# Performance work log

Hardware: AMD Instinct MI355X
Metric: run time of the kernel (lower is better)

## Reference

```python
import jax, jax.numpy as jnp
import numpy as np

E, H, N, HD, HID = 8, 12, 256, 64, 512  # experts, heads, tokens, head_dim, hidden_dim
B, K = 32, 2                             # batch, top_k


def setup_inputs() -> dict:
    key = jax.random.key(0)
    ks = jax.random.split(key, 7)
    w = lambda k, shp: (jax.random.uniform(k, shp, jnp.float32) * 2.0 - 1.0) * 0.05  # kaiming-uniform-ish
    return {
        "x": jax.random.normal(ks[0], (B, H, HD, N), jnp.float32),
        "expert_indices": jax.random.randint(ks[1], (B, H, K), 0, E),
        "expert_weights": jax.random.uniform(ks[2], (B, H, K), dtype=jnp.float32),
        "fc1_tok": w(ks[3], (E, H, HID, N)),
        "fc1_chan": w(ks[4], (E, H, HD, HD)),
        "fc1_bias": jnp.zeros((E, H, HD, HID), jnp.float32),
        "fc2_tok": w(ks[5], (E, H, N, HID)),
        "fc2_chan": w(ks[6], (E, H, HD, HD)),
        "fc2_bias": jnp.zeros((E, H, HD, N), jnp.float32),
    }


def reference(x, expert_indices, expert_weights, fc1_tok, fc1_chan, fc1_bias,
              fc2_tok, fc2_chan, fc2_bias):
    # x: (B,H,hd,N); expert_indices/weights: (B,H,K)
    Bh, Hh = x.shape[0], x.shape[1]
    hidx = jnp.arange(Hh)[None, :, None]           # (1,H,1) broadcasts with (B,H,K)
    gather = lambda p: p[expert_indices, hidx]     # -> (B,H,K, ...)
    w1t, w1c, b1 = gather(fc1_tok), gather(fc1_chan), gather(fc1_bias)
    w2t, w2c, b2 = gather(fc2_tok), gather(fc2_chan), gather(fc2_bias)
    # Layer 1: h = GELU(W1_chan @ x @ W1_tok^T + B1)   (token mix then channel mix)
    h = jnp.einsum('bhdn,bhken->bhkde', x, w1t)        # (B,H,K,hd,hid)
    h = jnp.einsum('bhkcd,bhkde->bhkce', w1c, h) + b1
    h = jax.nn.gelu(h, approximate=True)               # tanh approximation
    # Layer 2: out = W2_chan @ h @ W2_tok^T + B2
    o = jnp.einsum('bhkde,bhkne->bhkdn', h, w2t)       # (B,H,K,hd,N)
    o = jnp.einsum('bhkcd,bhkdn->bhkcn', w2c, o) + b2
    # Weighted combine over top_k
    return jnp.einsum('bhkdn,bhk->bhdn', o, expert_weights)
```

## Files before the change

kernel.cpp:

```cpp
#include <hip/hip_runtime.h>
#include <hip/hip_bf16.h>


namespace {
constexpr int NHEAD = 12, NTOK = 256, HDIM = 64, HIDD = 512, NBATCH = 32, TOPK = 2;
constexpr int NCHAIN = NBATCH * NHEAD * TOPK;
constexpr int NBH = NBATCH * NHEAD;
constexpr int NGROUP = 8 * NHEAD;

constexpr int P_T1 = HDIM * 2 + 16;
constexpr int T1_W = 64 * P_T1;
constexpr int SMA_TOTAL = 4 * T1_W;
constexpr int P_T3 = HDIM * 2 + 16;
constexpr int T3_W = 64 * P_T3;
constexpr int SMB_TOTAL = 4 * T3_W;

constexpr size_t SZ_H    = (size_t)NCHAIN * HDIM * HIDD;
constexpr size_t OFF_H   = 0;
constexpr size_t OFF_W1T = OFF_H + SZ_H;
constexpr size_t SZ_W1T  = (size_t)8 * NHEAD * HIDD * NTOK;
constexpr size_t OFF_W2T = OFF_W1T + SZ_W1T;
constexpr size_t SZ_W2T  = (size_t)8 * NHEAD * NTOK * HIDD;
constexpr size_t OFF_X   = OFF_W2T + SZ_W2T;
constexpr size_t SZ_X    = (size_t)NBATCH * NHEAD * HDIM * NTOK;
constexpr size_t OFF_B1  = OFF_X + SZ_X;
constexpr size_t SZ_B1   = (size_t)8 * NHEAD * HDIM * HIDD;
constexpr size_t OFF_B2  = OFF_B1 + SZ_B1;
constexpr size_t SZ_B2   = (size_t)8 * NHEAD * HDIM * NTOK;
constexpr size_t OFF_W1C = OFF_B2 + SZ_B2;
constexpr size_t SZ_W1C  = (size_t)8 * NHEAD * HDIM * HDIM;
constexpr size_t OFF_W2C = OFF_W1C + SZ_W1C;
constexpr size_t SZ_W2C  = (size_t)8 * NHEAD * HDIM * HDIM;
constexpr size_t TOTEL   = OFF_W2C + SZ_W2C;
constexpr size_t NEED    = TOTEL * 2 + (NCHAIN + NBH) * 4;

constexpr int NB_W1T = (int)(SZ_W1T / (16 * 256));
constexpr int NB_W2T = (int)(SZ_W2T / (16 * 512));
constexpr int NB_X   = (int)(SZ_X   / (16 * 256));
constexpr int NB_W1C = (int)(SZ_W1C / (16 * 64));
constexpr int NB_W2C = (int)(SZ_W2C / (16 * 64));
constexpr int NB_B1  = (int)(SZ_B1  / (16 * 512));
constexpr int NB_B2  = (int)(SZ_B2  / (16 * 256));
constexpr int NB_TOT = NB_W1T + NB_W2T + NB_X + NB_W1C + NB_W2C + NB_B1 + NB_B2;
}

typedef float f32x4 __attribute__((ext_vector_type(4)));
typedef short bf16x8 __attribute__((ext_vector_type(8)));
typedef short bf16x4 __attribute__((ext_vector_type(4)));

#define MFMA16(a, b, c) __builtin_amdgcn_mfma_f32_16x16x32_bf16((a), (b), (c), 0, 0, 0)

#define GLOAD_LDS16(g, l)                                                  \
  __builtin_amdgcn_global_load_lds(                                        \
      (const __attribute__((address_space(1))) unsigned int*)(g),          \
      (__attribute__((address_space(3))) unsigned int*)(l), 16, 0, 0)

__device__ __forceinline__ short f2bf(float f) {
  union { float f; unsigned u; } v; v.f = f;
  unsigned r = v.u + 0x7fffu + ((v.u >> 16) & 1u);
  return (short)(r >> 16);
}

__device__ __forceinline__ bf16x8 ld_gfrag(const float* p) {
  float4 a = *(const float4*)p;
  float4 b = *(const float4*)(p + 4);
  bf16x8 r;
  r[0] = f2bf(a.x); r[1] = f2bf(a.y); r[2] = f2bf(a.z); r[3] = f2bf(a.w);
  r[4] = f2bf(b.x); r[5] = f2bf(b.y); r[6] = f2bf(b.z); r[7] = f2bf(b.w);
  return r;
}

__device__ __forceinline__ f32x4 bf4f(bf16x4 v) {
  f32x4 r;
  #pragma unroll
  for (int i = 0; i < 4; ++i) {
    union { unsigned u; float f; } t;
    t.u = ((unsigned)(unsigned short)v[i]) << 16;
    r[i] = t.f;
  }
  return r;
}

__device__ __forceinline__ float gelu_fast(float x) {
  float arg = -2.30220826f * x * __builtin_fmaf(0.044715f, x * x, 1.0f);
  float e = __builtin_amdgcn_exp2f(arg);
  return x * __builtin_amdgcn_rcpf(1.0f + e);
}

__device__ __forceinline__ int xcd_chunk(int bx, int nwg) {
  return (bx & 7) * (nwg >> 3) + (bx >> 3);
}

__device__ __forceinline__ int swz8(int c)  { return c ^ (((c >> 4) & 3) << 1); }

__global__ __launch_bounds__(256) void prepack_sort_kernel(
    const float* __restrict__ w1t, const float* __restrict__ w2t,
    const float* __restrict__ x, const float* __restrict__ w1c,
    const float* __restrict__ w2c, const float* __restrict__ b1,
    const float* __restrict__ b2, short* __restrict__ wsb,
    const int* __restrict__ eidx, int* __restrict__ order, int* __restrict__ order2) {
  if (blockIdx.x == 0) {
    __shared__ int keys[NCHAIN];
    __shared__ int keys2[NBH];
    __shared__ int cnt[NGROUP + 1];
    __shared__ int cnt2[NGROUP + 1];
    const int t = threadIdx.x;
    for (int i = t; i <= NGROUP; i += 256) { cnt[i] = 0; cnt2[i] = 0; }
    __syncthreads();
    for (int i = t; i < NCHAIN; i += 256) {
      int h = (i >> 1) % NHEAD;
      int key = eidx[i] * NHEAD + h;
      keys[i] = key;
      atomicAdd(&cnt[key + 1], 1);
    }
    for (int i = t; i < NBH; i += 256) {
      int h = i % NHEAD;
      int key = eidx[i * TOPK] * NHEAD + h;
      keys2[i] = key;
      atomicAdd(&cnt2[key + 1], 1);
    }
    __syncthreads();
    if (t == 0) for (int i = 1; i <= NGROUP; ++i) cnt[i] += cnt[i - 1];
    if (t == 1) for (int i = 1; i <= NGROUP; ++i) cnt2[i] += cnt2[i - 1];
    __syncthreads();
    for (int i = t; i < NCHAIN; i += 256) {
      int pos = atomicAdd(&cnt[keys[i]], 1);
      order[pos] = i;
    }
    for (int i = t; i < NBH; i += 256) {
      int pos = atomicAdd(&cnt2[keys2[i]], 1);
      order2[pos] = i;
    }
    __syncthreads();
  }

  __shared__ __align__(16) float tilef[8192];
  short* tile = (short*)tilef;

  const int w64 = (threadIdx.x >> 6) * 64;
  const int lane = threadIdx.x & 63;

  for (int band = blockIdx.x; band < NB_TOT; band += gridDim.x) {
    const float* s; size_t dbase; int R, rcSh, tprSh; bool g8;
    int bb = band;
    if (bb < NB_W1T)                 { s = w1t; dbase = OFF_W1T; R = 256; rcSh = 6; tprSh = 3; g8 = true; }
    else if ((bb -= NB_W1T) < NB_W2T){ s = w2t; dbase = OFF_W2T; R = 512; rcSh = 7; tprSh = 4; g8 = true; }
    else if ((bb -= NB_W2T) < NB_X)  { s = x;   dbase = OFF_X;   R = 256; rcSh = 6; tprSh = 3; g8 = true; }
    else if ((bb -= NB_X) < NB_W1C)  { s = w1c; dbase = OFF_W1C; R = 64;  rcSh = 4; tprSh = 1; g8 = true; }
    else if ((bb -= NB_W1C) < NB_W2C){ s = w2c; dbase = OFF_W2C; R = 64;  rcSh = 4; tprSh = 1; g8 = true; }
    else if ((bb -= NB_W2C) < NB_B1) { s = b1;  dbase = OFF_B1;  R = 512; rcSh = 7; tprSh = 5; g8 = false; }
    else                             { bb -= NB_B1; s = b2; dbase = OFF_B2; R = 256; rcSh = 6; tprSh = 4; g8 = false; }

    const size_t eloff = (size_t)bb * 16 * R;

    if (g8) {
      const int nc = 4 * R;
      const float* bs = s + eloff;
      for (int c0 = w64; c0 < nc; c0 += 256) {
        const int c = c0 + lane;
        const int row = c >> rcSh, cir = c & ((1 << rcSh) - 1);
        const float* g = bs + (((size_t)row << rcSh) + (cir ^ (row & 7))) * 4;
        GLOAD_LDS16(g, tilef + (size_t)c0 * 4);
      }
      __syncthreads();

      const int n8 = (16 * R) / 8;
      for (int l8 = threadIdx.x; l8 < n8; l8 += 256) {
        const int frag = l8 >> 6, l6 = l8 & 63;
        const int c8 = ((frag & ((1 << tprSh) - 1)) << 2) + (l6 >> 4);
        const int r  = ((frag >> tprSh) << 4) + (l6 & 15);
        const int ch0 = (r << rcSh) + ((2 * c8) ^ (r & 7));
        const int ch1 = (r << rcSh) + ((2 * c8 + 1) ^ (r & 7));
        f32x4 a = *(const f32x4*)(tilef + ch0 * 4);
        f32x4 b = *(const f32x4*)(tilef + ch1 * 4);
        bf16x8 v;
        #pragma unroll
        for (int i = 0; i < 4; ++i) { v[i] = f2bf(a[i]); v[4 + i] = f2bf(b[i]); }
        *(bf16x8*)(wsb + dbase + eloff + (size_t)l8 * 8) = v;
      }
    } else {
      const int n8 = (16 * R) / 8;
      for (int l8 = threadIdx.x; l8 < n8; l8 += 256) {
        const int l = l8 * 8;
        const int r = l >> rcSh >> 2, c = l & (R - 1);
        bf16x8 v = ld_gfrag(s + eloff + l);
        #pragma unroll
        for (int q = 0; q < 2; ++q) {
          const int e4 = (c >> 2) + q;
          const int chunk = (e4 >> 2) * 64 + (e4 & 3) * 16 + r;
          bf16x4 p;
          #pragma unroll
          for (int i = 0; i < 4; ++i) p[i] = v[q * 4 + i];
          *(bf16x4*)(tile + swz8(chunk) * 4) = p;
        }
      }
      __syncthreads();
      for (int l8 = threadIdx.x; l8 < n8; l8 += 256) {
        const int l4 = l8 * 2;
        bf16x8 v;
        bf16x4 a = *(const bf16x4*)(tile + swz8(l4) * 4);
        bf16x4 b = *(const bf16x4*)(tile + swz8(l4 + 1) * 4);
        #pragma unroll
        for (int i = 0; i < 4; ++i) { v[i] = a[i]; v[4 + i] = b[i]; }
        *(bf16x8*)(wsb + dbase + eloff + (size_t)l8 * 8) = v;
      }
    }
    __syncthreads();
  }
}

template <bool PP>
__global__ __launch_bounds__(256) void mixer_h_kernel(
    const float* __restrict__ x, const int* __restrict__ eidx,
    const float* __restrict__ w1t, const float* __restrict__ w1c, const float* __restrict__ b1,
    const short* __restrict__ wsb, const int* __restrict__ order, short* __restrict__ hws) {
  __shared__ __align__(16) char smem[SMA_TOTAL];
  const int L = xcd_chunk(blockIdx.x, NCHAIN * 2);
  const int sid = L >> 1, eblk = L & 1;
  const int bhk = PP ? order[sid] : sid;
  const int h = (bhk >> 1) % NHEAD;
  const int tid = threadIdx.x, w = tid >> 6, lane = tid & 63, lr = lane & 15, lg = lane >> 4;

  const int e = eidx[bhk];
  const size_t eh = (size_t)e * NHEAD + h;
  short* H = hws + (size_t)bhk * HDIM * HIDD;

  const int e0 = eblk * 256 + w * 64;
  const int et0 = e0 >> 4;
  const int ks0B = e0 >> 5;

  const short* W1Tp = wsb + OFF_W1T + (eh << 17);
  const short* Xp   = wsb + OFF_X + ((size_t)(bhk >> 1) << 14);
  const short* W1Cp = wsb + OFF_W1C + (eh << 12);
  const short* B1p  = wsb + OFF_B1 + (eh << 15);

  f32x4 acc1[4][4];
  #pragma unroll
  for (int et = 0; et < 4; ++et)
    #pragma unroll
    for (int dt = 0; dt < 4; ++dt) acc1[et][dt] = (f32x4){0.f, 0.f, 0.f, 0.f};
  #pragma unroll
  for (int ks = 0; ks < 8; ++ks) {
    bf16x8 wfr[4];
    #pragma unroll
    for (int et = 0; et < 4; ++et) {
      if (PP) wfr[et] = *(const bf16x8*)(W1Tp + (size_t)(((et0 + et) * 8 + ks) * 512) + lane * 8);
      else    wfr[et] = ld_gfrag(w1t + eh * HIDD * NTOK +
                                 (size_t)(e0 + et * 16 + lr) * NTOK + ks * 32 + lg * 8);
    }
    #pragma unroll
    for (int dt = 0; dt < 4; ++dt) {
      bf16x8 xfr;
      if (PP) xfr = *(const bf16x8*)(Xp + (size_t)((dt * 8 + ks) * 512) + lane * 8);
      else    xfr = ld_gfrag(x + (size_t)(bhk >> 1) * HDIM * NTOK +
                             (size_t)(dt * 16 + lr) * NTOK + ks * 32 + lg * 8);
      #pragma unroll
      for (int et = 0; et < 4; ++et) acc1[et][dt] = MFMA16(xfr, wfr[et], acc1[et][dt]);
    }
  }

  char* t1 = smem + w * T1_W;
  #pragma unroll
  for (int et = 0; et < 4; ++et)
    #pragma unroll
    for (int dt = 0; dt < 4; ++dt) {
      bf16x4 p;
      #pragma unroll
      for (int i = 0; i < 4; ++i) p[i] = f2bf(acc1[et][dt][i]);
      *(bf16x4*)(t1 + (et * 16 + lr) * P_T1 + (dt * 16 + lg * 4) * 2) = p;
    }

  f32x4 acc2[4][4];
  #pragma unroll
  for (int et = 0; et < 4; ++et)
    #pragma unroll
    for (int ct = 0; ct < 4; ++ct) {
      if (PP) {
        bf16x4 bb = *(const bf16x4*)(B1p + (size_t)((ct * 32 + et0 + et) * 256) + lane * 4);
        acc2[et][ct] = bf4f(bb);
      } else {
        acc2[et][ct] = *(const f32x4*)(b1 + eh * HDIM * HIDD +
                                       (size_t)(ct * 16 + lr) * HIDD + e0 + et * 16 + lg * 4);
      }
    }
  #pragma unroll
  for (int ks = 0; ks < 2; ++ks) {
    bf16x8 a[4];
    #pragma unroll
    for (int et = 0; et < 4; ++et)
      a[et] = *(const bf16x8*)(t1 + (et * 16 + lr) * P_T1 + (ks * 32 + lg * 8) * 2);
    #pragma unroll
    for (int ct = 0; ct < 4; ++ct) {
      bf16x8 bfr;
      if (PP) bfr = *(const bf16x8*)(W1Cp + (size_t)((ct * 2 + ks) * 512) + lane * 8);
      else    bfr = ld_gfrag(w1c + eh * HDIM * HDIM +
                             (size_t)(ct * 16 + lr) * HDIM + ks * 32 + lg * 8);
      #pragma unroll
      for (int et = 0; et < 4; ++et) acc2[et][ct] = MFMA16(a[et], bfr, acc2[et][ct]);
    }
  }

  #pragma unroll
  for (int et = 0; et < 4; ++et) {
    const int ksB = ks0B + (et >> 1);
    const int lgB = (et & 1) * 2 + (lg >> 1);
    #pragma unroll
    for (int ct = 0; ct < 4; ++ct) {
      bf16x4 g;
      #pragma unroll
      for (int i = 0; i < 4; ++i) g[i] = f2bf(gelu_fast(acc2[et][ct][i]));
      if (PP) {
        *(bf16x4*)(H + (size_t)((ct * 16 + ksB) * 512) + (lgB * 16 + lr) * 8 + (lg & 1) * 4) = g;
      } else {
        *(bf16x4*)(H + (size_t)(ct * 16 + lr) * HIDD + e0 + et * 16 + lg * 4) = g;
      }
    }
  }
}

template <bool PP>
__global__ __launch_bounds__(256) void mixer_out_kernel(
    const int* __restrict__ eidx, const float* __restrict__ ewt,
    const float* __restrict__ w2t, const float* __restrict__ w2c, const float* __restrict__ b2,
    const short* __restrict__ wsb, const int* __restrict__ order2,
    const short* __restrict__ hws, float* __restrict__ out) {
  __shared__ __align__(16) char smem[SMB_TOTAL];
  const int L = xcd_chunk(blockIdx.x, NBH * 2);
  const int sid = L >> 1, nhalf = L & 1;
  const int bh = PP ? order2[sid] : sid;
  const int h = bh % NHEAD;
  const int tid = threadIdx.x, w = tid >> 6, lane = tid & 63, lr = lane & 15, lg = lane >> 4;
  const int kk = w >> 1, wq = w & 1;
  const int nb = nhalf * 128 + wq * 64;
  const int nt0 = nb >> 4;
  char* t3 = smem + w * T3_W;
  float* OUT = out + (size_t)bh * HDIM * NTOK;

  const int e = eidx[bh * TOPK + kk];
  const float wk = ewt[bh * TOPK + kk];
  const size_t eh = (size_t)e * NHEAD + h;
  const short* Hk = hws + (size_t)(bh * TOPK + kk) * HDIM * HIDD;
  const short* W2Tp = wsb + OFF_W2T + (eh << 17);
  const short* W2Cp = wsb + OFF_W2C + (eh << 12);
  const short* B2p  = wsb + OFF_B2 + (eh << 14);

  f32x4 acc3[4][4];
  #pragma unroll
  for (int ct = 0; ct < 4; ++ct)
    #pragma unroll
    for (int nt = 0; nt < 4; ++nt) acc3[ct][nt] = (f32x4){0.f, 0.f, 0.f, 0.f};
  #pragma unroll 4
  for (int ks = 0; ks < 16; ++ks) {
    bf16x8 a[4];
    #pragma unroll
    for (int ct = 0; ct < 4; ++ct) {
      if (PP) a[ct] = *(const bf16x8*)(Hk + (size_t)((ct * 16 + ks) * 512) + lane * 8);
      else    a[ct] = *(const bf16x8*)(Hk + (size_t)(ct * 16 + lr) * HIDD + ks * 32 + lg * 8);
    }
    #pragma unroll
    for (int nt = 0; nt < 4; ++nt) {
      bf16x8 bfr;
      if (PP) bfr = *(const bf16x8*)(W2Tp + (size_t)(((nt0 + nt) * 16 + ks) * 512) + lane * 8);
      else    bfr = ld_gfrag(w2t + eh * NTOK * HIDD +
                             (size_t)(nb + nt * 16 + lr) * HIDD + ks * 32 + lg * 8);
      #pragma unroll
      for (int ct = 0; ct < 4; ++ct) acc3[ct][nt] = MFMA16(a[ct], bfr, acc3[ct][nt]);
    }
  }

  #pragma unroll
  for (int ct = 0; ct < 4; ++ct)
    #pragma unroll
    for (int nt = 0; nt < 4; ++nt) {
      bf16x4 p;
      #pragma unroll
      for (int i = 0; i < 4; ++i) p[i] = f2bf(acc3[ct][nt][i]);
      *(bf16x4*)(t3 + (nt * 16 + lr) * P_T3 + (ct * 16 + lg * 4) * 2) = p;
    }

  f32x4 acc4[4][4];
  #pragma unroll
  for (int nt = 0; nt < 4; ++nt)
    #pragma unroll
    for (int ct = 0; ct < 4; ++ct) acc4[nt][ct] = (f32x4){0.f, 0.f, 0.f, 0.f};
  #pragma unroll
  for (int ks = 0; ks < 2; ++ks) {
    bf16x8 a[4];
    #pragma unroll
    for (int nt = 0; nt < 4; ++nt)
      a[nt] = *(const bf16x8*)(t3 + (nt * 16 + lr) * P_T3 + (ks * 32 + lg * 8) * 2);
    #pragma unroll
    for (int ct = 0; ct < 4; ++ct) {
      bf16x8 bfr;
      if (PP) bfr = *(const bf16x8*)(W2Cp + (size_t)((ct * 2 + ks) * 512) + lane * 8);
      else    bfr = ld_gfrag(w2c + eh * HDIM * HDIM +
                             (size_t)(ct * 16 + lr) * HDIM + ks * 32 + lg * 8);
      #pragma unroll
      for (int nt = 0; nt < 4; ++nt) acc4[nt][ct] = MFMA16(a[nt], bfr, acc4[nt][ct]);
    }
  }

  #pragma unroll
  for (int nt = 0; nt < 4; ++nt)
    #pragma unroll
    for (int cot = 0; cot < 4; ++cot) {
      f32x4 bb;
      if (PP) bb = bf4f(*(const bf16x4*)(B2p + (size_t)((cot * 16 + nt0 + nt) * 256) + lane * 4));
      else    bb = *(const f32x4*)(b2 + eh * HDIM * NTOK +
                                   (size_t)(cot * 16 + lr) * NTOK + nb + nt * 16 + lg * 4);
      #pragma unroll
      for (int i = 0; i < 4; ++i) acc4[nt][cot][i] = wk * (acc4[nt][cot][i] + bb[i]);
    }

  __syncthreads();

  if (kk == 1) {
    float* comb = (float*)(smem + wq * 16384);
    #pragma unroll
    for (int nt = 0; nt < 4; ++nt)
      #pragma unroll
      for (int cot = 0; cot < 4; ++cot) {
        const int co = cot * 16 + lr;
        #pragma unroll
        for (int i = 0; i < 4; ++i)
          comb[(nt * 16 + lg * 4 + i) * 64 + co] = acc4[nt][cot][i];
      }
  }
  __syncthreads();

  if (kk == 0) {
    const float* comb = (const float*)(smem + wq * 16384);
    #pragma unroll
    for (int nt = 0; nt < 4; ++nt)
      #pragma unroll
      for (int cot = 0; cot < 4; ++cot) {
        const int co = cot * 16 + lr;
        const int n0 = nb + nt * 16 + lg * 4;
        f32x4 v;
        #pragma unroll
        for (int i = 0; i < 4; ++i)
          v[i] = acc4[nt][cot][i] + comb[(nt * 16 + lg * 4 + i) * 64 + co];
        *(f32x4*)(OUT + (size_t)co * NTOK + n0) = v;
      }
  }
}

extern "C" void kernel_launch(void* const* d_in, const int* in_sizes, int n_in,
                              void* d_out, int out_size, void* d_ws, size_t ws_size,
                              hipStream_t stream) {
  const float* x   = (const float*)d_in[0];
  const int*   ei  = (const int*)d_in[1];
  const float* ew  = (const float*)d_in[2];
  const float* w1t = (const float*)d_in[3];
  const float* w1c = (const float*)d_in[4];
  const float* b1  = (const float*)d_in[5];
  const float* w2t = (const float*)d_in[6];
  const float* w2c = (const float*)d_in[7];
  const float* b2  = (const float*)d_in[8];
  float* out = (float*)d_out;
  short* wsb = (short*)d_ws;
  short* hws = wsb + OFF_H;
  int* order  = (int*)(wsb + TOTEL);
  int* order2 = order + NCHAIN;

  if (ws_size >= NEED) {
    prepack_sort_kernel<<<dim3(2048), dim3(256), 0, stream>>>(
        w1t, w2t, x, w1c, w2c, b1, b2, wsb, ei, order, order2);
    mixer_h_kernel<true><<<dim3(NCHAIN * 2), dim3(256), 0, stream>>>(
        x, ei, w1t, w1c, b1, wsb, order, hws);
    mixer_out_kernel<true><<<dim3(NBH * 2), dim3(256), 0, stream>>>(
        ei, ew, w2t, w2c, b2, wsb, order2, hws, out);
  } else {
    mixer_h_kernel<false><<<dim3(NCHAIN * 2), dim3(256), 0, stream>>>(
        x, ei, w1t, w1c, b1, wsb, order, hws);
    mixer_out_kernel<false><<<dim3(NBH * 2), dim3(256), 0, stream>>>(
        ei, ew, w2t, w2c, b2, wsb, order2, hws, out);
  }
}
```

Measured before the change: 130.9 us.

## Overlap layer-2 weight prepacking with layer-1 compute inside mixer_h kernel

Splits the prepack kernel so it converts only the layer-1 operands (w1t, x, w1c, b1). The layer-2 conversions (w2t, w2c, b2) move into extra blocks of the first mixer kernel: 8 of every 32 blocks do conversion bands while the other 24 compute H. This shortens the serial prepack stage and hides the layer-2 conversion behind layer-1 compute. In exchange, the mixer grid now holds 2048 blocks, and conversion blocks compete with compute blocks for bandwidth and CU slots.

```diff
diff --git a/kernel.cpp b/kernel.cpp
--- a/kernel.cpp
+++ b/kernel.cpp
@@ -34,14 +34,15 @@
 constexpr size_t TOTEL   = OFF_W2C + SZ_W2C;
 constexpr size_t NEED    = TOTEL * 2 + (NCHAIN + NBH) * 4;
 
-constexpr int NB_W1T = (int)(SZ_W1T / (16 * 256));
-constexpr int NB_W2T = (int)(SZ_W2T / (16 * 512));
-constexpr int NB_X   = (int)(SZ_X   / (16 * 256));
-constexpr int NB_W1C = (int)(SZ_W1C / (16 * 64));
-constexpr int NB_W2C = (int)(SZ_W2C / (16 * 64));
-constexpr int NB_B1  = (int)(SZ_B1  / (16 * 512));
-constexpr int NB_B2  = (int)(SZ_B2  / (16 * 256));
-constexpr int NB_TOT = NB_W1T + NB_W2T + NB_X + NB_W1C + NB_W2C + NB_B1 + NB_B2;
+constexpr int NA_W1T = (int)(SZ_W1T / (16 * 256));
+constexpr int NA_X   = (int)(SZ_X   / (16 * 256));
+constexpr int NA_W1C = (int)(SZ_W1C / (16 * 64));
+constexpr int NA_B1  = (int)(SZ_B1  / (16 * 512));
+constexpr int NA_TOT = NA_W1T + NA_X + NA_W1C + NA_B1;
+constexpr int NBB_W2T = (int)(SZ_W2T / (16 * 512));
+constexpr int NBB_W2C = (int)(SZ_W2C / (16 * 64));
+constexpr int NBB_B2  = (int)(SZ_B2  / (16 * 256));
+constexpr int NBB_TOT = NBB_W2T + NBB_W2C + NBB_B2;
 }
 
 typedef float f32x4 __attribute__((ext_vector_type(4)));
@@ -93,11 +94,71 @@
 
 __device__ __forceinline__ int swz8(int c)  { return c ^ (((c >> 4) & 3) << 1); }
 
-__global__ __launch_bounds__(256) void prepack_sort_kernel(
-    const float* __restrict__ w1t, const float* __restrict__ w2t,
-    const float* __restrict__ x, const float* __restrict__ w1c,
-    const float* __restrict__ w2c, const float* __restrict__ b1,
-    const float* __restrict__ b2, short* __restrict__ wsb,
+__device__ __forceinline__ void do_band_g8(
+    const float* s, short* wsb, size_t dbase, size_t eloff, int R, int rcSh,
+    int tprSh, float* tilef, int tid) {
+  const int w64 = (tid >> 6) * 64, lane = tid & 63;
+  const int nc = 4 * R;
+  const float* bs = s + eloff;
+  for (int c0 = w64; c0 < nc; c0 += 256) {
+    const int c = c0 + lane;
+    const int row = c >> rcSh, cir = c & ((1 << rcSh) - 1);
+    const float* g = bs + (((size_t)row << rcSh) + (cir ^ (row & 7))) * 4;
+    GLOAD_LDS16(g, tilef + (size_t)c0 * 4);
+  }
+  __syncthreads();
+  const int n8 = (16 * R) / 8;
+  for (int l8 = tid; l8 < n8; l8 += 256) {
+    const int frag = l8 >> 6, l6 = l8 & 63;
+    const int c8 = ((frag & ((1 << tprSh) - 1)) << 2) + (l6 >> 4);
+    const int r  = ((frag >> tprSh) << 4) + (l6 & 15);
+    const int ch0 = (r << rcSh) + ((2 * c8) ^ (r & 7));
+    const int ch1 = (r << rcSh) + ((2 * c8 + 1) ^ (r & 7));
+    f32x4 a = *(const f32x4*)(tilef + ch0 * 4);
+    f32x4 b = *(const f32x4*)(tilef + ch1 * 4);
+    bf16x8 v;
+    #pragma unroll
+    for (int i = 0; i < 4; ++i) { v[i] = f2bf(a[i]); v[4 + i] = f2bf(b[i]); }
+    *(bf16x8*)(wsb + dbase + eloff + (size_t)l8 * 8) = v;
+  }
+  __syncthreads();
+}
+
+__device__ __forceinline__ void do_band_bias(
+    const float* s, short* wsb, size_t dbase, size_t eloff, int R,
+    short* tile, int tid) {
+  const int n8 = (16 * R) / 8;
+  for (int l8 = tid; l8 < n8; l8 += 256) {
+    const int l = l8 * 8;
+    const int r = l / R, c = l % R;
+    bf16x8 v = ld_gfrag(s + eloff + l);
+    #pragma unroll
+    for (int q = 0; q < 2; ++q) {
+      const int e4 = (c >> 2) + q;
+      const int chunk = (e4 >> 2) * 64 + (e4 & 3) * 16 + r;
+      bf16x4 p;
+      #pragma unroll
+      for (int i = 0; i < 4; ++i) p[i] = v[q * 4 + i];
+      *(bf16x4*)(tile + swz8(chunk) * 4) = p;
+    }
+  }
+  __syncthreads();
+  for (int l8 = tid; l8 < n8; l8 += 256) {
+    const int l4 = l8 * 2;
+    bf16x8 v;
+    bf16x4 a = *(const bf16x4*)(tile + swz8(l4) * 4);
+    bf16x4 b = *(const bf16x4*)(tile + swz8(l4 + 1) * 4);
+    #pragma unroll
+    for (int i = 0; i < 4; ++i) { v[i] = a[i]; v[4 + i] = b[i]; }
+    *(bf16x8*)(wsb + dbase + eloff + (size_t)l8 * 8) = v;
+  }
+  __syncthreads();
+}
+
+__global__ __launch_bounds__(256) void prepackA_sort_kernel(
+    const float* __restrict__ w1t, const float* __restrict__ x,
+    const float* __restrict__ w1c, const float* __restrict__ b1,
+    short* __restrict__ wsb,
     const int* __restrict__ eidx, int* __restrict__ order, int* __restrict__ order2) {
   if (blockIdx.x == 0) {
     __shared__ int keys[NCHAIN];
@@ -137,85 +198,52 @@
   __shared__ __align__(16) float tilef[8192];
   short* tile = (short*)tilef;
 
-  const int w64 = (threadIdx.x >> 6) * 64;
-  const int lane = threadIdx.x & 63;
-
-  for (int band = blockIdx.x; band < NB_TOT; band += gridDim.x) {
-    const float* s; size_t dbase; int R, rcSh, tprSh; bool g8;
+  for (int band = blockIdx.x; band < NA_TOT; band += gridDim.x) {
     int bb = band;
-    if (bb < NB_W1T)                 { s = w1t; dbase = OFF_W1T; R = 256; rcSh = 6; tprSh = 3; g8 = true; }
-    else if ((bb -= NB_W1T) < NB_W2T){ s = w2t; dbase = OFF_W2T; R = 512; rcSh = 7; tprSh = 4; g8 = true; }
-    else if ((bb -= NB_W2T) < NB_X)  { s = x;   dbase = OFF_X;   R = 256; rcSh = 6; tprSh = 3; g8 = true; }
-    else if ((bb -= NB_X) < NB_W1C)  { s = w1c; dbase = OFF_W1C; R = 64;  rcSh = 4; tprSh = 1; g8 = true; }
-    else if ((bb -= NB_W1C) < NB_W2C){ s = w2c; dbase = OFF_W2C; R = 64;  rcSh = 4; tprSh = 1; g8 = true; }
-    else if ((bb -= NB_W2C) < NB_B1) { s = b1;  dbase = OFF_B1;  R = 512; rcSh = 7; tprSh = 5; g8 = false; }
-    else                             { bb -= NB_B1; s = b2; dbase = OFF_B2; R = 256; rcSh = 6; tprSh = 4; g8 = false; }
-
-    const size_t eloff = (size_t)bb * 16 * R;
-
-    if (g8) {
-      const int nc = 4 * R;
-      const float* bs = s + eloff;
-      for (int c0 = w64; c0 < nc; c0 += 256) {
-        const int c = c0 + lane;
-        const int row = c >> rcSh, cir = c & ((1 << rcSh) - 1);
-        const float* g = bs + (((size_t)row << rcSh) + (cir ^ (row & 7))) * 4;
-        GLOAD_LDS16(g, tilef + (size_t)c0 * 4);
-      }
-      __syncthreads();
-
-      const int n8 = (16 * R) / 8;
-      for (int l8 = threadIdx.x; l8 < n8; l8 += 256) {
-        const int frag = l8 >> 6, l6 = l8 & 63;
-        const int c8 = ((frag & ((1 << tprSh) - 1)) << 2) + (l6 >> 4);
-        const int r  = ((frag >> tprSh) << 4) + (l6 & 15);
-        const int ch0 = (r << rcSh) + ((2 * c8) ^ (r & 7));
-        const int ch1 = (r << rcSh) + ((2 * c8 + 1) ^ (r & 7));
-        f32x4 a = *(const f32x4*)(tilef + ch0 * 4);
-        f32x4 b = *(const f32x4*)(tilef + ch1 * 4);
-        bf16x8 v;
-        #pragma unroll
-        for (int i = 0; i < 4; ++i) { v[i] = f2bf(a[i]); v[4 + i] = f2bf(b[i]); }
-        *(bf16x8*)(wsb + dbase + eloff + (size_t)l8 * 8) = v;
-      }
+    if (bb < NA_W1T) {
+      do_band_g8(w1t, wsb, OFF_W1T, (size_t)bb * 16 * 256, 256, 6, 3, tilef, threadIdx.x);
+    } else if ((bb -= NA_W1T) < NA_X) {
+      do_band_g8(x, wsb, OFF_X, (size_t)bb * 16 * 256, 256, 6, 3, tilef, threadIdx.x);
+    } else if ((bb -= NA_X) < NA_W1C) {
+      do_band_g8(w1c, wsb, OFF_W1C, (size_t)bb * 16 * 64, 64, 4, 1, tilef, threadIdx.x);
     } else {
-      const int n8 = (16 * R) / 8;
-      for (int l8 = threadIdx.x; l8 < n8; l8 += 256) {
-        const int l = l8 * 8;
-        const int r = l >> rcSh >> 2, c = l & (R - 1);
-        bf16x8 v = ld_gfrag(s + eloff + l);
-        #pragma unroll
-        for (int q = 0; q < 2; ++q) {
-          const int e4 = (c >> 2) + q;
-          const int chunk = (e4 >> 2) * 64 + (e4 & 3) * 16 + r;
-          bf16x4 p;
-          #pragma unroll
-          for (int i = 0; i < 4; ++i) p[i] = v[q * 4 + i];
-          *(bf16x4*)(tile + swz8(chunk) * 4) = p;
-        }
-      }
-      __syncthreads();
-      for (int l8 = threadIdx.x; l8 < n8; l8 += 256) {
-        const int l4 = l8 * 2;
-        bf16x8 v;
-        bf16x4 a = *(const bf16x4*)(tile + swz8(l4) * 4);
-        bf16x4 b = *(const bf16x4*)(tile + swz8(l4 + 1) * 4);
-        #pragma unroll
-        for (int i = 0; i < 4; ++i) { v[i] = a[i]; v[4 + i] = b[i]; }
-        *(bf16x8*)(wsb + dbase + eloff + (size_t)l8 * 8) = v;
-      }
-    }
-    __syncthreads();
+      bb -= NA_W1C;
+      do_band_bias(b1, wsb, OFF_B1, (size_t)bb * 16 * 512, 512, tile, threadIdx.x);
+    }
   }
 }
 
 template <bool PP>
-__global__ __launch_bounds__(256) void mixer_h_kernel(
+__global__ __launch_bounds__(256) void mixer_h_cvt_kernel(
     const float* __restrict__ x, const int* __restrict__ eidx,
     const float* __restrict__ w1t, const float* __restrict__ w1c, const float* __restrict__ b1,
-    const short* __restrict__ wsb, const int* __restrict__ order, short* __restrict__ hws) {
+    const float* __restrict__ w2t, const float* __restrict__ w2c, const float* __restrict__ b2,
+    short* __restrict__ wsb, const int* __restrict__ order, short* __restrict__ hws) {
   __shared__ __align__(16) char smem[SMA_TOTAL];
-  const int L = xcd_chunk(blockIdx.x, NCHAIN * 2);
+  const int bx = blockIdx.x;
+  const int sub = bx & 31;
+
+  if (sub >= 24) {
+    if (!PP) return;
+    float* tilef = (float*)smem;
+    short* tile = (short*)smem;
+    const int cidx = (bx >> 5) * 8 + (sub - 24);
+    for (int band = cidx; band < NBB_TOT; band += 512) {
+      int bb = band;
+      if (bb < NBB_W2T) {
+        do_band_g8(w2t, wsb, OFF_W2T, (size_t)bb * 16 * 512, 512, 7, 4, tilef, threadIdx.x);
+      } else if ((bb -= NBB_W2T) < NBB_W2C) {
+        do_band_g8(w2c, wsb, OFF_W2C, (size_t)bb * 16 * 64, 64, 4, 1, tilef, threadIdx.x);
+      } else {
+        bb -= NBB_W2C;
+        do_band_bias(b2, wsb, OFF_B2, (size_t)bb * 16 * 256, 256, tile, threadIdx.x);
+      }
+    }
+    return;
+  }
+
+  const int aidx = (bx >> 5) * 24 + sub;
+  const int L = xcd_chunk(aidx, NCHAIN * 2);
   const int sid = L >> 1, eblk = L & 1;
   const int bhk = PP ? order[sid] : sid;
   const int h = (bhk >> 1) % NHEAD;
@@ -464,15 +492,15 @@
   int* order2 = order + NCHAIN;
 
   if (ws_size >= NEED) {
-    prepack_sort_kernel<<<dim3(2048), dim3(256), 0, stream>>>(
-        w1t, w2t, x, w1c, w2c, b1, b2, wsb, ei, order, order2);
-    mixer_h_kernel<true><<<dim3(NCHAIN * 2), dim3(256), 0, stream>>>(
-        x, ei, w1t, w1c, b1, wsb, order, hws);
+    prepackA_sort_kernel<<<dim3(2048), dim3(256), 0, stream>>>(
+        w1t, x, w1c, b1, wsb, ei, order, order2);
+    mixer_h_cvt_kernel<true><<<dim3(2048), dim3(256), 0, stream>>>(
+        x, ei, w1t, w1c, b1, w2t, w2c, b2, wsb, order, hws);
     mixer_out_kernel<true><<<dim3(NBH * 2), dim3(256), 0, stream>>>(
         ei, ew, w2t, w2c, b2, wsb, order2, hws, out);
   } else {
-    mixer_h_kernel<false><<<dim3(NCHAIN * 2), dim3(256), 0, stream>>>(
-        x, ei, w1t, w1c, b1, wsb, order, hws);
+    mixer_h_cvt_kernel<false><<<dim3(2048), dim3(256), 0, stream>>>(
+        x, ei, w1t, w1c, b1, w2t, w2c, b2, wsb, order, hws);
     mixer_out_kernel<false><<<dim3(NBH * 2), dim3(256), 0, stream>>>(
         ei, ew, w2t, w2c, b2, wsb, order2, hws, out);
   }
```

New measurement: 137.5 us. 1.05x slower.
